# Kernel optimization log

Measured on AMD Instinct MI355X. Metric: run time of the kernel, lower is better.

Reference implementation:

```python
import jax, jax.numpy as jnp
import numpy as np

T = 36  # num_frames


def box_cxcywh_to_xyxy(b):
    cx, cy, w, h = jnp.split(b, 4, axis=-1)
    return jnp.concatenate([cx - 0.5 * w, cy - 0.5 * h, cx + 0.5 * w, cy + 0.5 * h], axis=-1)


def multi_iou(b1, b2):
    # b1: [Q,1,T,4], b2: [1,N,T,4], xyxy -> iou [Q,N,T]
    lt = jnp.maximum(b1[..., :2], b2[..., :2])
    rb = jnp.minimum(b1[..., 2:], b2[..., 2:])
    wh = jnp.clip(rb - lt, 0.0)
    inter = wh[..., 0] * wh[..., 1]
    a1 = (b1[..., 2] - b1[..., 0]) * (b1[..., 3] - b1[..., 1])
    a2 = (b2[..., 2] - b2[..., 0]) * (b2[..., 3] - b2[..., 1])
    union = a1 + a2 - inter
    return inter / union


def setup_inputs() -> dict:
    key = jax.random.key(0)
    k1, k2, k3, k4, k5, k6 = jax.random.split(key, 6)
    Q, N, C = 2048, 128, 42
    return {
        "pred_logits": jax.random.normal(k1, (T * Q, C), dtype=jnp.float32),
        "pred_boxes": jax.random.uniform(k2, (T * Q, 4), dtype=jnp.float32),
        "tgt_labels": jax.random.randint(k3, (N * T,), 0, C - 1),
        "tgt_boxes": jax.random.uniform(k4, (N * T, 4), dtype=jnp.float32),
        "tgt_valid": jax.random.randint(k5, (N * T,), 0, 2, dtype=jnp.int32),
        "tgt_original_valid": jax.random.randint(k6, (N * T,), 0, 2, dtype=jnp.int32),
    }


def reference(pred_logits, pred_boxes, tgt_labels, tgt_boxes, tgt_valid, tgt_original_valid):
    # Cost-matrix computation of SoftMaxHungarianMatcher (cost_class=cost_bbox=cost_giou=1,
    # use_giou=False, use_l1_distance_sum=False). The scipy linear_sum_assignment step is
    # CPU-serial / non-tensor and excluded; output is the [Q,N] cost fed to it.
    C = pred_logits.shape[-1]
    Q = pred_logits.shape[0] // T
    N = tgt_labels.shape[0] // T
    num_classes = C - 1  # background index

    probs = jax.nn.softmax(pred_logits, axis=-1).reshape(T, Q, C).transpose(1, 0, 2)  # [Q,T,C]
    boxes = pred_boxes.reshape(T, Q, 4).transpose(1, 0, 2)                            # [Q,T,4]
    tboxes = tgt_boxes.reshape(N, T, 4)
    valid = tgt_valid.reshape(N, T).astype(probs.dtype)                               # [N,T]
    ovalid = tgt_original_valid.reshape(N, T)
    ids = jnp.where(ovalid == 0, num_classes, tgt_labels.reshape(N, T))               # [N,T]

    denom = valid.sum(-1)  # [N] (per-instance count of valid frames)

    # class cost: -mean_t p(q, t, ids[n,t]) over valid frames
    gathered = probs[:, jnp.arange(T)[None, :], ids]                                  # [Q,N,T]
    class_cost = -(gathered * valid).sum(-1) / denom                                  # [Q,N]

    # bbox L1 cost: mean over (valid frames, 4 coords)
    l1 = jnp.abs(boxes[:, None] - tboxes[None]).mean(-1)                              # [Q,N,T]
    bbox_cost = (l1 * valid).sum(-1) / denom                                          # [Q,N]

    # IoU cost: -mean_t iou over valid frames
    iou = multi_iou(box_cxcywh_to_xyxy(boxes)[:, None], box_cxcywh_to_xyxy(tboxes)[None])
    iou_cost = -(iou * valid).sum(-1) / denom                                         # [Q,N]

    return class_cost + bbox_cost + iou_cost
```

## Files before the change

### kernel.cpp

```cpp
#include <hip/hip_runtime.h>
#include <hip/hip_bf16.h>


constexpr int T = 36;
constexpr int Q = 2048;
constexpr int C = 42;
constexpr int N = 128;

__global__ __launch_bounds__(256) void softmax_transpose_kernel(
    const float* __restrict__ logits, float* __restrict__ P2) {
  constexpr int QB = 64;
  constexpr int LS = C + 1;

  __shared__ float tile[QB * LS];
  __shared__ float s_max[4 * QB];
  __shared__ float s_sum[4 * QB];
  __shared__ float s_rinv[QB];

  const int t = blockIdx.y;
  const int q0 = blockIdx.x * QB;
  const int tid = threadIdx.x;

  const float* src = logits + ((size_t)t * Q + q0) * C;
  for (int i = tid; i < QB * C; i += 256) {
    int r = i / C, c = i % C;
    tile[r * LS + c] = src[i];
  }
  __syncthreads();

  const int part = tid >> 6;
  const int row = tid & 63;
  const int c0 = (part < 2) ? part * 11 : 22 + (part - 2) * 10;
  const int c1 = (part < 2) ? c0 + 11 : c0 + 10;

  float m = -1e30f;
  for (int c = c0; c < c1; ++c) m = fmaxf(m, tile[row * LS + c]);
  s_max[part * QB + row] = m;
  __syncthreads();

  m = fmaxf(fmaxf(s_max[row], s_max[QB + row]),
            fmaxf(s_max[2 * QB + row], s_max[3 * QB + row]));
  float s = 0.f;
  for (int c = c0; c < c1; ++c) {
    float e = __expf(tile[row * LS + c] - m);
    tile[row * LS + c] = e;
    s += e;
  }
  s_sum[part * QB + row] = s;
  __syncthreads();

  if (part == 0) {
    float stot = s_sum[row] + s_sum[QB + row] + s_sum[2 * QB + row] +
                 s_sum[3 * QB + row];
    s_rinv[row] = 1.f / stot;
  }
  __syncthreads();

  for (int i = tid; i < QB * C; i += 256) {
    int c = i >> 6;
    int r = i & 63;
    P2[(size_t)(t * C + c) * Q + q0 + r] = tile[r * LS + c] * s_rinv[r];
  }
}

__global__ __launch_bounds__(512) void cost_kernel(
    const float* __restrict__ P2, const float* __restrict__ pred_boxes,
    const int* __restrict__ labels, const float* __restrict__ tboxes,
    const int* __restrict__ valid, const int* __restrict__ ovalid,
    float* __restrict__ out) {
  constexpr int NB = 4;
  constexpr int RS = NB + 1;

  const int q0 = blockIdx.x * 64;
  const int n0 = blockIdx.y * NB;
  const int tid = threadIdx.x;
  const int lane = tid & 63;
  const int sub = (tid >> 6) & 3;
  const int half = tid >> 8;
  const int q = q0 + lane;

  __shared__ float4 s_tb[NB * T];
  __shared__ int s_idv[NB * T];
  __shared__ float s_rden[NB];
  __shared__ float s_res[2 * 64 * RS];

  for (int i = tid; i < NB * T; i += 512) {
    int n = n0 + i / T;
    int t = i % T;
    int g = n * T + t;
    s_idv[i] = ((ovalid[g] == 0) ? (C - 1) : labels[g]) | (valid[g] << 8);
    s_tb[i] = ((const float4*)tboxes)[g];
  }
  if (tid < NB) {
    int n = n0 + tid;
    int s = 0;
    for (int t = 0; t < T; ++t) s += valid[n * T + t];
    s_rden[tid] = 1.f / (float)s;
  }
  __syncthreads();

  float acc = 0.f;
  const float* probs_base = P2 + q;
  const int t_begin = half * (T / 2);
  const int t_end = t_begin + (T / 2);

  for (int t = t_begin; t < t_end; ++t) {
    int pk = s_idv[sub * T + t];
    if (pk & 0x100) {
      float4 pb = ((const float4*)pred_boxes)[t * Q + q];
      float4 tb = s_tb[sub * T + t];
      int id = pk & 0xff;
      float p = probs_base[(size_t)(t * C + id) * Q];

      float l1 = 0.25f * (fabsf(pb.x - tb.x) + fabsf(pb.y - tb.y) +
                          fabsf(pb.z - tb.z) + fabsf(pb.w - tb.w));
      float px1 = pb.x - 0.5f * pb.z, py1 = pb.y - 0.5f * pb.w;
      float px2 = pb.x + 0.5f * pb.z, py2 = pb.y + 0.5f * pb.w;
      float tx1 = tb.x - 0.5f * tb.z, ty1 = tb.y - 0.5f * tb.w;
      float tx2 = tb.x + 0.5f * tb.z, ty2 = tb.y + 0.5f * tb.w;
      float iw = fmaxf(fminf(px2, tx2) - fmaxf(px1, tx1), 0.f);
      float ih = fmaxf(fminf(py2, ty2) - fmaxf(py1, ty1), 0.f);
      float inter = iw * ih;
      float uni = pb.z * pb.w + tb.z * tb.w - inter;
      acc += l1 - p - inter / uni;
    }
  }

  s_res[half * (64 * RS) + lane * RS + sub] = acc;
  __syncthreads();
  if (half == 0) {
    float tot = (acc + s_res[64 * RS + lane * RS + sub]) * s_rden[sub];
    s_res[lane * RS + sub] = tot;
  }
  __syncthreads();

  if (tid < 64) {
    float4 o;
    o.x = s_res[tid * RS + 0];
    o.y = s_res[tid * RS + 1];
    o.z = s_res[tid * RS + 2];
    o.w = s_res[tid * RS + 3];
    *(float4*)(out + (size_t)(q0 + tid) * N + n0) = o;
  }
}

extern "C" void kernel_launch(void* const* d_in, const int* in_sizes, int n_in,
                              void* d_out, int out_size, void* d_ws, size_t ws_size,
                              hipStream_t stream) {
  const float* logits = (const float*)d_in[0];
  const float* pboxes = (const float*)d_in[1];
  const int* labels = (const int*)d_in[2];
  const float* tboxes = (const float*)d_in[3];
  const int* valid = (const int*)d_in[4];
  const int* ovalid = (const int*)d_in[5];
  float* out = (float*)d_out;

  float* P2 = (float*)d_ws;

  dim3 g1(Q / 64, T);
  softmax_transpose_kernel<<<g1, 256, 0, stream>>>(logits, P2);

  dim3 g2(Q / 64, N / 4);
  cost_kernel<<<g2, 512, 0, stream>>>(P2, pboxes, labels, tboxes, valid, ovalid, out);
}
```

Measured before the change: 87.90 us.

## Fuse softmax into cost computation with per-frame atomic accumulation

The probability matrix is no longer written to and re-read from global memory. Each block now computes the softmax for one frame and 64 queries, then evaluates the class, L1 and IoU terms for all 128 targets. Each term is atomically added into an [N,Q] workspace, which a finalize kernel transposes and scales by the per-target valid count. This removes the transposed probability traffic but adds a zeroing kernel, about 36-way atomic contention per output element and an extra pass over the output.

```diff
diff --git a/kernel.cpp b/kernel.cpp
--- a/kernel.cpp
+++ b/kernel.cpp
@@ -7,140 +7,124 @@
 constexpr int C = 42;
 constexpr int N = 128;
 
-__global__ __launch_bounds__(256) void softmax_transpose_kernel(
-    const float* __restrict__ logits, float* __restrict__ P2) {
-  constexpr int QB = 64;
+__global__ __launch_bounds__(256) void zero_ws_kernel(float4* __restrict__ ws2) {
+  ws2[blockIdx.x * 256 + threadIdx.x] = make_float4(0.f, 0.f, 0.f, 0.f);
+}
+
+__global__ __launch_bounds__(256) void fused_cost_kernel(
+    const float* __restrict__ logits, const float* __restrict__ pred_boxes,
+    const int* __restrict__ labels, const float* __restrict__ tboxes,
+    const int* __restrict__ valid, const int* __restrict__ ovalid,
+    float* __restrict__ ws2) {
   constexpr int LS = C + 1;
 
-  __shared__ float tile[QB * LS];
-  __shared__ float s_max[4 * QB];
-  __shared__ float s_sum[4 * QB];
-  __shared__ float s_rinv[QB];
+  __shared__ float tile[64 * LS];
+  __shared__ float s_max[4 * 64];
+  __shared__ float s_sum[4 * 64];
+  __shared__ float s_rinv[64];
+  __shared__ float4 s_tb[N];
+  __shared__ int s_idv[N];
 
   const int t = blockIdx.y;
-  const int q0 = blockIdx.x * QB;
+  const int q0 = blockIdx.x * 64;
   const int tid = threadIdx.x;
+  const int lane = tid & 63;
+  const int sub = tid >> 6;
+  const int q = q0 + lane;
 
   const float* src = logits + ((size_t)t * Q + q0) * C;
-  for (int i = tid; i < QB * C; i += 256) {
-    int r = i / C, c = i % C;
-    tile[r * LS + c] = src[i];
+  for (int i = tid; i < 64 * C; i += 256) {
+    tile[(i / C) * LS + (i % C)] = src[i];
+  }
+  if (tid < N) {
+    int g = tid * T + t;
+    s_idv[tid] = ((ovalid[g] == 0) ? (C - 1) : labels[g]) | (valid[g] << 8);
+    s_tb[tid] = ((const float4*)tboxes)[g];
   }
   __syncthreads();
 
-  const int part = tid >> 6;
-  const int row = tid & 63;
+  const int part = sub;
+  const int row = lane;
   const int c0 = (part < 2) ? part * 11 : 22 + (part - 2) * 10;
   const int c1 = (part < 2) ? c0 + 11 : c0 + 10;
 
   float m = -1e30f;
   for (int c = c0; c < c1; ++c) m = fmaxf(m, tile[row * LS + c]);
-  s_max[part * QB + row] = m;
+  s_max[part * 64 + row] = m;
   __syncthreads();
 
-  m = fmaxf(fmaxf(s_max[row], s_max[QB + row]),
-            fmaxf(s_max[2 * QB + row], s_max[3 * QB + row]));
+  m = fmaxf(fmaxf(s_max[row], s_max[64 + row]),
+            fmaxf(s_max[128 + row], s_max[192 + row]));
   float s = 0.f;
   for (int c = c0; c < c1; ++c) {
     float e = __expf(tile[row * LS + c] - m);
     tile[row * LS + c] = e;
     s += e;
   }
-  s_sum[part * QB + row] = s;
+  s_sum[part * 64 + row] = s;
   __syncthreads();
 
   if (part == 0) {
-    float stot = s_sum[row] + s_sum[QB + row] + s_sum[2 * QB + row] +
-                 s_sum[3 * QB + row];
-    s_rinv[row] = 1.f / stot;
+    s_rinv[row] = 1.f / (s_sum[row] + s_sum[64 + row] + s_sum[128 + row] +
+                         s_sum[192 + row]);
   }
   __syncthreads();
 
-  for (int i = tid; i < QB * C; i += 256) {
-    int c = i >> 6;
-    int r = i & 63;
-    P2[(size_t)(t * C + c) * Q + q0 + r] = tile[r * LS + c] * s_rinv[r];
-  }
-}
+  const float rinv_l = s_rinv[lane];
 
-__global__ __launch_bounds__(512) void cost_kernel(
-    const float* __restrict__ P2, const float* __restrict__ pred_boxes,
-    const int* __restrict__ labels, const float* __restrict__ tboxes,
-    const int* __restrict__ valid, const int* __restrict__ ovalid,
-    float* __restrict__ out) {
-  constexpr int NB = 4;
-  constexpr int RS = NB + 1;
+  float4 pb = ((const float4*)pred_boxes)[t * Q + q];
+  const float px1 = pb.x - 0.5f * pb.z, py1 = pb.y - 0.5f * pb.w;
+  const float px2 = pb.x + 0.5f * pb.z, py2 = pb.y + 0.5f * pb.w;
+  const float pa = pb.z * pb.w;
 
-  const int q0 = blockIdx.x * 64;
-  const int n0 = blockIdx.y * NB;
-  const int tid = threadIdx.x;
-  const int lane = tid & 63;
-  const int sub = (tid >> 6) & 3;
-  const int half = tid >> 8;
-  const int q = q0 + lane;
-
-  __shared__ float4 s_tb[NB * T];
-  __shared__ int s_idv[NB * T];
-  __shared__ float s_rden[NB];
-  __shared__ float s_res[2 * 64 * RS];
-
-  for (int i = tid; i < NB * T; i += 512) {
-    int n = n0 + i / T;
-    int t = i % T;
-    int g = n * T + t;
-    s_idv[i] = ((ovalid[g] == 0) ? (C - 1) : labels[g]) | (valid[g] << 8);
-    s_tb[i] = ((const float4*)tboxes)[g];
-  }
-  if (tid < NB) {
-    int n = n0 + tid;
-    int s = 0;
-    for (int t = 0; t < T; ++t) s += valid[n * T + t];
-    s_rden[tid] = 1.f / (float)s;
-  }
-  __syncthreads();
-
-  float acc = 0.f;
-  const float* probs_base = P2 + q;
-  const int t_begin = half * (T / 2);
-  const int t_end = t_begin + (T / 2);
-
-  for (int t = t_begin; t < t_end; ++t) {
-    int pk = s_idv[sub * T + t];
+  for (int i = 0; i < 32; ++i) {
+    int n = i * 4 + sub;
+    int pk = s_idv[n];
     if (pk & 0x100) {
-      float4 pb = ((const float4*)pred_boxes)[t * Q + q];
-      float4 tb = s_tb[sub * T + t];
-      int id = pk & 0xff;
-      float p = probs_base[(size_t)(t * C + id) * Q];
-
+      float4 tb = s_tb[n];
+      float p = tile[lane * LS + (pk & 0xff)] * rinv_l;
       float l1 = 0.25f * (fabsf(pb.x - tb.x) + fabsf(pb.y - tb.y) +
                           fabsf(pb.z - tb.z) + fabsf(pb.w - tb.w));
-      float px1 = pb.x - 0.5f * pb.z, py1 = pb.y - 0.5f * pb.w;
-      float px2 = pb.x + 0.5f * pb.z, py2 = pb.y + 0.5f * pb.w;
       float tx1 = tb.x - 0.5f * tb.z, ty1 = tb.y - 0.5f * tb.w;
       float tx2 = tb.x + 0.5f * tb.z, ty2 = tb.y + 0.5f * tb.w;
       float iw = fmaxf(fminf(px2, tx2) - fmaxf(px1, tx1), 0.f);
       float ih = fmaxf(fminf(py2, ty2) - fmaxf(py1, ty1), 0.f);
       float inter = iw * ih;
-      float uni = pb.z * pb.w + tb.z * tb.w - inter;
-      acc += l1 - p - inter / uni;
+      float uni = pa + tb.z * tb.w - inter;
+      float term = l1 - p - inter / uni;
+      unsafeAtomicAdd(&ws2[(size_t)n * Q + q], term);
     }
   }
+}
 
-  s_res[half * (64 * RS) + lane * RS + sub] = acc;
-  __syncthreads();
-  if (half == 0) {
-    float tot = (acc + s_res[64 * RS + lane * RS + sub]) * s_rden[sub];
-    s_res[lane * RS + sub] = tot;
+__global__ __launch_bounds__(256) void finalize_kernel(
+    const float* __restrict__ ws2, const int* __restrict__ valid,
+    float* __restrict__ out) {
+  __shared__ float s_t[64 * 65];
+  __shared__ float s_rd[64];
+
+  const int q0 = blockIdx.x * 64;
+  const int n0 = blockIdx.y * 64;
+  const int tid = threadIdx.x;
+
+  if (tid < 64) {
+    int n = n0 + tid;
+    const int4* vp = (const int4*)(valid + n * T);
+    int s = 0;
+    for (int k = 0; k < T / 4; ++k) {
+      int4 v = vp[k];
+      s += v.x + v.y + v.z + v.w;
+    }
+    s_rd[tid] = 1.f / (float)s;
+  }
+  for (int i = tid; i < 64 * 64; i += 256) {
+    int nl = i >> 6, ql = i & 63;
+    s_t[nl * 65 + ql] = ws2[(size_t)(n0 + nl) * Q + q0 + ql];
   }
   __syncthreads();
-
-  if (tid < 64) {
-    float4 o;
-    o.x = s_res[tid * RS + 0];
-    o.y = s_res[tid * RS + 1];
-    o.z = s_res[tid * RS + 2];
-    o.w = s_res[tid * RS + 3];
-    *(float4*)(out + (size_t)(q0 + tid) * N + n0) = o;
+  for (int i = tid; i < 64 * 64; i += 256) {
+    int ql = i >> 6, nl = i & 63;
+    out[(size_t)(q0 + ql) * N + n0 + nl] = s_t[nl * 65 + ql] * s_rd[nl];
   }
 }
 
@@ -155,11 +139,14 @@
   const int* ovalid = (const int*)d_in[5];
   float* out = (float*)d_out;
 
-  float* P2 = (float*)d_ws;
+  float* ws2 = (float*)d_ws;
 
-  dim3 g1(Q / 64, T);
-  softmax_transpose_kernel<<<g1, 256, 0, stream>>>(logits, P2);
+  zero_ws_kernel<<<(N * Q / 4) / 256, 256, 0, stream>>>((float4*)ws2);
 
-  dim3 g2(Q / 64, N / 4);
-  cost_kernel<<<g2, 512, 0, stream>>>(P2, pboxes, labels, tboxes, valid, ovalid, out);
+  dim3 g(Q / 64, T);
+  fused_cost_kernel<<<g, 256, 0, stream>>>(logits, pboxes, labels, tboxes,
+                                           valid, ovalid, ws2);
+
+  dim3 gf(Q / 64, N / 64);
+  finalize_kernel<<<gf, 256, 0, stream>>>(ws2, valid, out);
 }
```

After: 95.22 us. 1.08x slower.
